# Kernel optimization log

Measured on AMD Instinct MI355X. Metric: run time of the kernel, lower is better.

The kernel has to match this reference:

```python
import jax, jax.numpy as jnp
import numpy as np

B, S, D, H, IT, V = 2, 1024, 1024, 8, 28, 50257
DH = D // H
EPS = jnp.float32(1.1920929e-07)  # torch RMSNorm default eps = finfo(float32).eps


def _rmsnorm(x, w):
    # torch nn.RMSNorm: x * rsqrt(mean(x^2) + eps) * weight
    ms = jnp.mean(jnp.square(x), axis=-1, keepdims=True)
    return x * jax.lax.rsqrt(ms + EPS) * w


def setup_inputs() -> dict:
    key = jax.random.key(0)
    ks = jax.random.split(key, 8)
    s = 0.02
    tokens = jax.random.randint(ks[0], (B, S), 0, V)
    embed = jax.random.normal(ks[1], (V, D), dtype=jnp.float32) * s
    Wk = jax.random.normal(ks[2], (D, D), dtype=jnp.float32) * s
    Wv = jax.random.normal(ks[3], (D, D), dtype=jnp.float32) * s
    Ws = jax.random.normal(ks[4], (D, D), dtype=jnp.float32) * s
    Wo = jax.random.normal(ks[5], (D, D), dtype=jnp.float32) * s  # original zero-inits; randomized for a non-trivial baseline
    step_size = jnp.linspace(0.5, 0.1, IT, dtype=jnp.float32)
    norm_w = jnp.ones((IT, D), jnp.float32)   # per-iteration RMSNorm weight
    gamma = jnp.ones((IT, D), jnp.float32)
    beta = jnp.zeros((IT, D), jnp.float32)
    out_norm_w = jnp.ones((D,), jnp.float32)
    lm_head_w = jax.random.normal(ks[6], (V, D), dtype=jnp.float32) * s
    return dict(tokens=tokens, embed=embed, Wk=Wk, Wv=Wv, Ws=Ws, Wo=Wo,
                step_size=step_size, norm_w=norm_w, gamma=gamma, beta=beta,
                out_norm_w=out_norm_w, lm_head_w=lm_head_w)


def _forward(tokens, embed, Wk, Wv, Ws, Wo, step_size, norm_w, gamma, beta, out_norm_w, lm_head_w):
    b, s = tokens.shape
    causal = jnp.tril(jnp.ones((s, s), dtype=bool))  # allow j <= i
    scale = 1.0 / np.sqrt(DH)

    def compute_force(h):
        k = (h @ Wk.T).reshape(b, s, H, DH)
        v = (h @ Wv.T).reshape(b, s, H, DH)
        energy = jnp.einsum('bihd,bjhd->bhij', k, k) * scale
        logits = jnp.where(causal, -energy, -jnp.inf)  # softmax(-energy) with causal masking
        w = jax.nn.softmax(logits, axis=-1)
        pairwise = jnp.einsum('bhij,bjhd->bihd', w, v).reshape(b, s, D)
        return (pairwise + h @ Ws.T) @ Wo.T

    def step(x, p):
        st, nw, g, bb = p
        h = _rmsnorm(x, nw) * g + bb
        return x + compute_force(h) * st, None

    x0 = embed[tokens].astype(jnp.float32)
    x, _ = jax.lax.scan(jax.checkpoint(step), x0, (step_size, norm_w, gamma, beta))
    x = _rmsnorm(x, out_norm_w)
    return x @ lm_head_w.T  # [B, S, V] logits


def reference(tokens, embed, Wk, Wv, Ws, Wo, step_size, norm_w, gamma, beta, out_norm_w, lm_head_w):
    return _forward(tokens, embed, Wk, Wv, Ws, Wo, step_size, norm_w, gamma, beta, out_norm_w, lm_head_w)
```

## Files before the change

kernel.cpp:

```cpp
#include <hip/hip_runtime.h>
#include <cstdint>
#include <cstddef>

#define S_   1024
#define D_   1024
#define H_   8
#define DH_  128
#define IT_  28
#define V_   50257
#define B_   2
#define ROWS 2048
#define EPS_ 1.1920929e-07f

typedef unsigned short u16;
typedef __attribute__((ext_vector_type(8))) short s8v;
typedef __attribute__((ext_vector_type(4))) float f4v;

static __device__ __forceinline__ void gload16(const void* g, void* l) {
  __builtin_amdgcn_global_load_lds((__attribute__((address_space(1))) void*)(g),
                                   (__attribute__((address_space(3))) void*)(l), 16, 0, 0);
}

static __device__ __forceinline__ u16 f2bf(float f) {
  union { float f; uint32_t u; } v; v.f = f;
  return (u16)((v.u + 0x7FFFu + ((v.u >> 16) & 1u)) >> 16);
}

static __device__ __forceinline__ float wave_sum(float v) {
#pragma unroll
  for (int o = 32; o > 0; o >>= 1) v += __shfl_xor(v, o, 64);
  return v;
}

__device__ __constant__ int IT_TAB[40] = {
  15,15,15,15, 14,14,14, 13,13,13, 12,12,12, 11,11,11,
  10,10, 9,9, 8,8, 7,7, 6, 5, 4, 3,
  14,10,6,2, 13,9,5,1, 12,8,4,0};
__device__ __constant__ int CH_TAB[40] = {
  0,1,2,3, 0,1,2, 0,1,2, 0,1,2, 0,1,2,
  0,1, 0,1, 0,1, 0,1, 0, 0, 0, 0,
  3,2,1,0, 3,2,1,0, 3,2,1,0};

__global__ __launch_bounds__(256) void k_embed(const int* __restrict__ tok,
                                               const float* __restrict__ emb,
                                               float* __restrict__ x) {
  const int row = blockIdx.x;
  const int t = tok[row];
  ((float4*)(x + (size_t)row * D_))[threadIdx.x] =
      ((const float4*)(emb + (size_t)t * D_))[threadIdx.x];
}

__global__ __launch_bounds__(256) void k_cvt(const float* __restrict__ w,
                                             u16* __restrict__ o, int n4) {
  const int idx = blockIdx.x * 256 + threadIdx.x;
  if (idx < n4) {
    const float4 f = ((const float4*)w)[idx];
    ushort4 u;
    u.x = f2bf(f.x); u.y = f2bf(f.y); u.z = f2bf(f.z); u.w = f2bf(f.w);
    ((ushort4*)o)[idx] = u;
  }
}

__global__ __launch_bounds__(256) void k_rmsnorm(const float* __restrict__ x,
                                                 const float* __restrict__ nw,
                                                 const float* __restrict__ g,
                                                 const float* __restrict__ bb,
                                                 u16* __restrict__ h) {
  const int row = blockIdx.x;
  const int tid = threadIdx.x;
  const float4 xv = ((const float4*)(x + (size_t)row * D_))[tid];
  float ss = xv.x*xv.x + xv.y*xv.y + xv.z*xv.z + xv.w*xv.w;
  ss = wave_sum(ss);
  __shared__ float red[4];
  const int lane = tid & 63, wid = tid >> 6;
  if (lane == 0) red[wid] = ss;
  __syncthreads();
  const float tot = red[0] + red[1] + red[2] + red[3];
  const float r = rsqrtf(tot * (1.0f / (float)D_) + EPS_);
  const float4 wv = ((const float4*)nw)[tid];
  float o[4];
  o[0] = xv.x * r * wv.x; o[1] = xv.y * r * wv.y;
  o[2] = xv.z * r * wv.z; o[3] = xv.w * r * wv.w;
  if (g) {
    const float4 gv = ((const float4*)g)[tid];
    const float4 bv = ((const float4*)bb)[tid];
    o[0] = o[0]*gv.x + bv.x; o[1] = o[1]*gv.y + bv.y;
    o[2] = o[2]*gv.z + bv.z; o[3] = o[3]*gv.w + bv.w;
  }
  ushort4 u;
  u.x = f2bf(o[0]); u.y = f2bf(o[1]); u.z = f2bf(o[2]); u.w = f2bf(o[3]);
  ((ushort4*)(h + (size_t)row * D_))[tid] = u;
}

template<int EPI, int SWAP>
__global__ __launch_bounds__(256) void k_gemm(const u16* __restrict__ A, int lda,
                                              const u16* __restrict__ Bm, int ldb,
                                              float* __restrict__ C, int ldc,
                                              int N, int K,
                                              const float* __restrict__ alphap, int aidx) {
  __shared__ u16 As[128 * 32];
  __shared__ u16 Bs[64 * 32];
  const int i0 = (SWAP ? blockIdx.x : blockIdx.y) * 128;
  const int j0 = (SWAP ? blockIdx.y : blockIdx.x) * 64;
  const int tid = threadIdx.x;
  const int lane = tid & 63, w = tid >> 6;
  const int wr = w >> 1, wc = w & 1;
  const int l15 = lane & 15, l4 = lane >> 4;
  const int ar = tid >> 2, ak = (tid & 3) << 3;
  int bj = j0 + ar; if (bj > N - 1) bj = N - 1;

  f4v acc[4][2];
#pragma unroll
  for (int m = 0; m < 4; ++m)
#pragma unroll
    for (int n = 0; n < 2; ++n) acc[m][n] = (f4v)0.0f;

  for (int k0 = 0; k0 < K; k0 += 32) {
    gload16(A + (size_t)(i0 + ar) * lda + k0 + ak, &As[(size_t)tid * 8]);
    gload16(A + (size_t)(i0 + ar + 64) * lda + k0 + ak, &As[((size_t)tid + 256) * 8]);
    gload16(Bm + (size_t)bj * ldb + k0 + ak, &Bs[(size_t)tid * 8]);
    __syncthreads();
    s8v a[4], b[2];
#pragma unroll
    for (int m = 0; m < 4; ++m)
      a[m] = *(const s8v*)&As[(wr * 64 + m * 16 + l15) * 32 + l4 * 8];
#pragma unroll
    for (int n = 0; n < 2; ++n)
      b[n] = *(const s8v*)&Bs[(wc * 32 + n * 16 + l15) * 32 + l4 * 8];
#pragma unroll
    for (int m = 0; m < 4; ++m)
#pragma unroll
      for (int n = 0; n < 2; ++n)
        acc[m][n] = __builtin_amdgcn_mfma_f32_16x16x32_bf16(a[m], b[n], acc[m][n], 0, 0, 0);
    __syncthreads();
  }

  const float alpha = alphap ? alphap[aidx] : 1.0f;
#pragma unroll
  for (int m = 0; m < 4; ++m) {
#pragma unroll
    for (int n = 0; n < 2; ++n) {
      const int i = i0 + wr * 64 + m * 16 + l4 * 4;
      const int j = j0 + wc * 32 + n * 16 + l15;
      const f4v v = acc[m][n];
      if (EPI == 0) {
        if (j < N) {
#pragma unroll
          for (int r = 0; r < 4; ++r) C[(size_t)(i + r) * ldc + j] = v[r];
        }
      } else {
#pragma unroll
        for (int r = 0; r < 4; ++r) C[(size_t)(i + r) * ldc + j] += alpha * v[r];
      }
    }
  }
}

__global__ __launch_bounds__(256) void k_gemm_qkv(const u16* __restrict__ A,
                                                  const u16* __restrict__ Wcat,
                                                  u16* __restrict__ kb,
                                                  u16* __restrict__ vt,
                                                  float* __restrict__ fb) {
  __shared__ u16 As[128 * 32];
  __shared__ u16 Bs[64 * 32];
  const int i0 = blockIdx.y * 128, j0 = blockIdx.x * 64;
  const int tid = threadIdx.x;
  const int lane = tid & 63, w = tid >> 6;
  const int wr = w >> 1, wc = w & 1;
  const int l15 = lane & 15, l4 = lane >> 4;
  const int ar = tid >> 2, ak = (tid & 3) << 3;

  f4v acc[4][2];
#pragma unroll
  for (int m = 0; m < 4; ++m)
#pragma unroll
    for (int n = 0; n < 2; ++n) acc[m][n] = (f4v)0.0f;

  for (int k0 = 0; k0 < D_; k0 += 32) {
    gload16(A + (size_t)(i0 + ar) * D_ + k0 + ak, &As[(size_t)tid * 8]);
    gload16(A + (size_t)(i0 + ar + 64) * D_ + k0 + ak, &As[((size_t)tid + 256) * 8]);
    gload16(Wcat + (size_t)(j0 + ar) * D_ + k0 + ak, &Bs[(size_t)tid * 8]);
    __syncthreads();
    s8v a[4], b[2];
#pragma unroll
    for (int m = 0; m < 4; ++m)
      a[m] = *(const s8v*)&As[(wr * 64 + m * 16 + l15) * 32 + l4 * 8];
#pragma unroll
    for (int n = 0; n < 2; ++n)
      b[n] = *(const s8v*)&Bs[(wc * 32 + n * 16 + l15) * 32 + l4 * 8];
#pragma unroll
    for (int m = 0; m < 4; ++m)
#pragma unroll
      for (int n = 0; n < 2; ++n)
        acc[m][n] = __builtin_amdgcn_mfma_f32_16x16x32_bf16(a[m], b[n], acc[m][n], 0, 0, 0);
    __syncthreads();
  }

#pragma unroll
  for (int m = 0; m < 4; ++m) {
#pragma unroll
    for (int n = 0; n < 2; ++n) {
      const int i = i0 + wr * 64 + m * 16 + l4 * 4;
      const int j = j0 + wc * 32 + n * 16 + l15;
      const int sel = j >> 10, jl = j & 1023;
      const f4v v = acc[m][n];
      if (sel == 0) {
#pragma unroll
        for (int r = 0; r < 4; ++r) kb[(size_t)(i + r) * D_ + jl] = f2bf(v[r]);
      } else if (sel == 1) {
        ushort4 p;
        p.x = f2bf(v[0]); p.y = f2bf(v[1]); p.z = f2bf(v[2]); p.w = f2bf(v[3]);
        *(ushort4*)&vt[((size_t)(i >> 10) * D_ + jl) * S_ + (i & 1023)] = p;
      } else {
#pragma unroll
        for (int r = 0; r < 4; ++r) fb[(size_t)(i + r) * D_ + jl] = v[r];
      }
    }
  }
}

__global__ __launch_bounds__(256) void k_attn_part(const u16* __restrict__ kb,
                                                   const u16* __restrict__ vt,
                                                   float* __restrict__ po,
                                                   float* __restrict__ pml,
                                                   float scale) {
  const int it = IT_TAB[blockIdx.x], ch = CH_TAB[blockIdx.x];
  const int z = blockIdx.y;
  const int b = z >> 3, h = z & 7;
  const u16* Kbh = kb + (size_t)b * S_ * D_ + h * DH_;
  const u16* Vth = vt + ((size_t)b * D_ + h * DH_) * S_;
  const int i0 = it * 64;
  const int jt0 = ch * 4;
  const int jtend = min(jt0 + 4, it + 1);
  __shared__ u16 Kj[64 * 128];
  __shared__ u16 Vj[128 * 64];
  __shared__ u16 Pl[4][16 * 64];
  const int tid = threadIdx.x;
  const int lane = tid & 63, w = tid >> 6;
  const int l15 = lane & 15, l4 = lane >> 4;

  s8v ka[4];
#pragma unroll
  for (int ks = 0; ks < 4; ++ks)
    ka[ks] = *(const s8v*)(Kbh + (size_t)(i0 + w * 16 + l15) * D_ + ks * 32 + l4 * 8);

  f4v acc_o[8];
#pragma unroll
  for (int n = 0; n < 8; ++n) acc_o[n] = (f4v)0.0f;
  float mrow[4], lrow[4];
#pragma unroll
  for (int r = 0; r < 4; ++r) { mrow[r] = -3.0e38f; lrow[r] = 0.f; }

  const int krow = tid >> 4, koff = (tid & 15) * 8;
  const int vrow = tid >> 3, voff = (tid & 7) * 8;

  for (int jt = jt0; jt < jtend; ++jt) {
    const int j0 = jt * 64;
#pragma unroll
    for (int p = 0; p < 4; ++p) {
      const int row = p * 16 + krow;
      gload16(Kbh + (size_t)(j0 + row) * D_ + (koff ^ ((row & 7) << 3)),
              &Kj[(size_t)(p * 256 + tid) * 8]);
    }
#pragma unroll
    for (int p = 0; p < 4; ++p) {
      const int row = p * 32 + vrow;
      gload16(Vth + (size_t)row * S_ + j0 + (voff ^ ((row & 7) << 3)),
              &Vj[(size_t)(p * 256 + tid) * 8]);
    }
    __syncthreads();

    f4v s[4];
#pragma unroll
    for (int n = 0; n < 4; ++n) s[n] = (f4v)0.0f;
#pragma unroll
    for (int ks = 0; ks < 4; ++ks) {
#pragma unroll
      for (int n = 0; n < 4; ++n) {
        const int row = n * 16 + l15;
        const s8v kf = *(const s8v*)&Kj[row * 128 + ((ks * 32 + l4 * 8) ^ ((row & 7) << 3))];
        s[n] = __builtin_amdgcn_mfma_f32_16x16x32_bf16(ka[ks], kf, s[n], 0, 0, 0);
      }
    }

    float pv[4][4], tmax[4];
#pragma unroll
    for (int r = 0; r < 4; ++r) tmax[r] = -3.0e38f;
#pragma unroll
    for (int n = 0; n < 4; ++n) {
      const int j = j0 + n * 16 + l15;
#pragma unroll
      for (int r = 0; r < 4; ++r) {
        const int i = i0 + w * 16 + l4 * 4 + r;
        const float lg = (j <= i) ? (-scale * s[n][r]) : -3.0e38f;
        pv[n][r] = lg;
        tmax[r] = fmaxf(tmax[r], lg);
      }
    }
#pragma unroll
    for (int r = 0; r < 4; ++r) {
#pragma unroll
      for (int o = 8; o > 0; o >>= 1) tmax[r] = fmaxf(tmax[r], __shfl_xor(tmax[r], o, 64));
    }
    float es[4];
#pragma unroll
    for (int r = 0; r < 4; ++r) {
      const float mn = fmaxf(mrow[r], tmax[r]);
      es[r] = __expf(mrow[r] - mn);
      mrow[r] = mn;
    }
    float psum[4] = {0.f, 0.f, 0.f, 0.f};
#pragma unroll
    for (int n = 0; n < 4; ++n) {
#pragma unroll
      for (int r = 0; r < 4; ++r) {
        const float p = __expf(pv[n][r] - mrow[r]);
        pv[n][r] = p;
        psum[r] += p;
      }
    }
#pragma unroll
    for (int r = 0; r < 4; ++r) {
#pragma unroll
      for (int o = 8; o > 0; o >>= 1) psum[r] += __shfl_xor(psum[r], o, 64);
      lrow[r] = lrow[r] * es[r] + psum[r];
    }
#pragma unroll
    for (int n = 0; n < 8; ++n) {
      f4v t = acc_o[n];
      t[0] *= es[0]; t[1] *= es[1]; t[2] *= es[2]; t[3] *= es[3];
      acc_o[n] = t;
    }

    u16* P = Pl[w];
#pragma unroll
    for (int n = 0; n < 4; ++n) {
#pragma unroll
      for (int r = 0; r < 4; ++r) {
        const int row = l4 * 4 + r;
        P[row * 64 + ((n * 16 + l15) ^ ((row & 7) << 3))] = f2bf(pv[n][r]);
      }
    }
    __syncthreads();
    s8v pa[2];
#pragma unroll
    for (int kp = 0; kp < 2; ++kp)
      pa[kp] = *(const s8v*)&P[l15 * 64 + ((kp * 32 + l4 * 8) ^ ((l15 & 7) << 3))];

#pragma unroll
    for (int kp = 0; kp < 2; ++kp) {
#pragma unroll
      for (int n = 0; n < 8; ++n) {
        const int d = n * 16 + l15;
        const s8v vf = *(const s8v*)&Vj[d * 64 + ((kp * 32 + l4 * 8) ^ ((d & 7) << 3))];
        acc_o[n] = __builtin_amdgcn_mfma_f32_16x16x32_bf16(pa[kp], vf, acc_o[n], 0, 0, 0);
      }
    }
    __syncthreads();
  }

  const int slot = (z * 16 + it) * 4 + ch;
  float* O = po + (size_t)slot * (64 * 128);
#pragma unroll
  for (int n = 0; n < 8; ++n) {
#pragma unroll
    for (int r = 0; r < 4; ++r)
      O[(w * 16 + l4 * 4 + r) * 128 + n * 16 + l15] = acc_o[n][r];
  }
  if (l15 == 0) {
#pragma unroll
    for (int r = 0; r < 4; ++r) {
      const int row = w * 16 + l4 * 4 + r;
      pml[(size_t)slot * 128 + row] = mrow[r];
      pml[(size_t)slot * 128 + 64 + row] = lrow[r];
    }
  }
}

__global__ __launch_bounds__(256) void k_attn_merge(const float* __restrict__ po,
                                                    const float* __restrict__ pml,
                                                    const float* __restrict__ fb,
                                                    u16* __restrict__ fbh) {
  const int it = blockIdx.x, z = blockIdx.y;
  const int b = z >> 3, h = z & 7;
  const int nch = (it >> 2) + 1;
  const int row = threadIdx.x >> 2;
  const int cseg = (threadIdx.x & 3) * 32;
  const int base = (z * 16 + it) * 4;

  float ms = -3.0e38f, mv[4], lv[4];
#pragma unroll
  for (int c = 0; c < 4; ++c)
    if (c < nch) {
      mv[c] = pml[(size_t)(base + c) * 128 + row];
      lv[c] = pml[(size_t)(base + c) * 128 + 64 + row];
      ms = fmaxf(ms, mv[c]);
    }
  float ls = 0.f, fac[4];
#pragma unroll
  for (int c = 0; c < 4; ++c)
    if (c < nch) { fac[c] = __expf(mv[c] - ms); ls += lv[c] * fac[c]; }
  const float inv = 1.0f / ls;

  float4 o[8];
#pragma unroll
  for (int q = 0; q < 8; ++q) o[q] = make_float4(0.f, 0.f, 0.f, 0.f);
#pragma unroll
  for (int c = 0; c < 4; ++c)
    if (c < nch) {
      const float4* Oc = (const float4*)(po + (size_t)(base + c) * (64 * 128) + row * 128 + cseg);
      const float f = fac[c];
#pragma unroll
      for (int q = 0; q < 8; ++q) {
        const float4 t = Oc[q];
        o[q].x += t.x * f; o[q].y += t.y * f; o[q].z += t.z * f; o[q].w += t.w * f;
      }
    }

  const size_t gidx = ((size_t)(b * S_ + it * 64 + row)) * D_ + h * DH_ + cseg;
  const float4* F = (const float4*)(fb + gidx);
  u16* out = fbh + gidx;
#pragma unroll
  for (int q = 0; q < 8; ++q) {
    const float4 fv = F[q];
    ushort4 u;
    u.x = f2bf(fv.x + o[q].x * inv);
    u.y = f2bf(fv.y + o[q].y * inv);
    u.z = f2bf(fv.z + o[q].z * inv);
    u.w = f2bf(fv.w + o[q].w * inv);
    *(ushort4*)(out + q * 4) = u;
  }
}

extern "C" void kernel_launch(void* const* d_in, const int* in_sizes, int n_in,
                              void* d_out, int out_size, void* d_ws, size_t ws_size,
                              hipStream_t stream) {
  const int*   tok = (const int*)  d_in[0];
  const float* emb = (const float*)d_in[1];
  const float* Wk  = (const float*)d_in[2];
  const float* Wv  = (const float*)d_in[3];
  const float* Ws  = (const float*)d_in[4];
  const float* Wo  = (const float*)d_in[5];
  const float* stp = (const float*)d_in[6];
  const float* nw  = (const float*)d_in[7];
  const float* gam = (const float*)d_in[8];
  const float* bet = (const float*)d_in[9];
  const float* onw = (const float*)d_in[10];
  const float* lmw = (const float*)d_in[11];
  float* out = (float*)d_out;

  uint8_t* wsb = (uint8_t*)d_ws;
  float* x   = (float*)wsb;  wsb += (size_t)ROWS * D_ * 4;
  u16* hb    = (u16*)wsb;    wsb += (size_t)ROWS * D_ * 2;
  u16* kb    = (u16*)wsb;    wsb += (size_t)ROWS * D_ * 2;
  u16* vt    = (u16*)wsb;    wsb += (size_t)ROWS * D_ * 2;
  float* fb  = (float*)wsb;  wsb += (size_t)ROWS * D_ * 4;
  u16* fbh   = (u16*)wsb;    wsb += (size_t)ROWS * D_ * 2;
  u16* Wcat  = (u16*)wsb;    wsb += (size_t)3 * D_ * D_ * 2;
  u16* Wob   = (u16*)wsb;    wsb += (size_t)D_ * D_ * 2;
  float* po  = (float*)wsb;  wsb += (size_t)1024 * 64 * 128 * 4;
  float* pml = (float*)wsb;  wsb += (size_t)1024 * 128 * 4;
  u16* Wlm   = (u16*)wsb;    wsb += (size_t)V_ * D_ * 2;

  const float scale = 0.08838834764831845f;
  const int n4 = D_ * D_ / 4;

  k_cvt<<<1024, 256, 0, stream>>>(Wk, Wcat, n4);
  k_cvt<<<1024, 256, 0, stream>>>(Wv, Wcat + (size_t)D_ * D_, n4);
  k_cvt<<<1024, 256, 0, stream>>>(Ws, Wcat + (size_t)2 * D_ * D_, n4);
  k_cvt<<<1024, 256, 0, stream>>>(Wo, Wob, n4);
  k_embed<<<ROWS, 256, 0, stream>>>(tok, emb, x);

  for (int it = 0; it < IT_; ++it) {
    k_rmsnorm<<<ROWS, 256, 0, stream>>>(x, nw + (size_t)it * D_,
                                        gam + (size_t)it * D_, bet + (size_t)it * D_, hb);
    k_gemm_qkv<<<dim3(48, 16), 256, 0, stream>>>(hb, Wcat, kb, vt, fb);
    k_attn_part<<<dim3(40, 16), 256, 0, stream>>>(kb, vt, po, pml, scale);
    k_attn_merge<<<dim3(16, 16), 256, 0, stream>>>(po, pml, fb, fbh);
    k_gemm<1, 0><<<dim3(16, 16), 256, 0, stream>>>(fbh, D_, Wob, D_, x, D_, D_, D_, stp, it);
  }

  k_rmsnorm<<<ROWS, 256, 0, stream>>>(x, onw, nullptr, nullptr, hb);

  k_cvt<<<(V_ * 256 + 255) / 256, 256, 0, stream>>>(lmw, Wlm, V_ * D_ / 4);
  k_gemm<0, 1><<<dim3(16, (V_ + 63) / 64), 256, 0, stream>>>(hb, D_, Wlm, D_, out, V_, V_, D_,
                                                             nullptr, 0);
}
```

Before: 2.927 ms.

## Widen LM-head GEMM tile to 128 columns and remap blocks per XCD

Adds a template parameter so the LM-head GEMM computes 128x128 tiles instead of 128x64. This halves how often the A operand is reloaded and doubles the MFMA work per LDS sync. For the swapped LM-head launch, it also remaps block IDs so consecutive tiles, which share the same B rows, land on the same XCD for better L2 reuse. The cost is more accumulator registers per thread and fewer blocks in the grid.

```diff
diff --git a/kernel.cpp b/kernel.cpp
--- a/kernel.cpp
+++ b/kernel.cpp
@@ -92,45 +92,57 @@
   ((ushort4*)(h + (size_t)row * D_))[tid] = u;
 }
 
-template<int EPI, int SWAP>
+template<int EPI, int SWAP, int NB>
 __global__ __launch_bounds__(256) void k_gemm(const u16* __restrict__ A, int lda,
                                               const u16* __restrict__ Bm, int ldb,
                                               float* __restrict__ C, int ldc,
                                               int N, int K,
                                               const float* __restrict__ alphap, int aidx) {
   __shared__ u16 As[128 * 32];
-  __shared__ u16 Bs[64 * 32];
-  const int i0 = (SWAP ? blockIdx.x : blockIdx.y) * 128;
-  const int j0 = (SWAP ? blockIdx.y : blockIdx.x) * 64;
+  __shared__ u16 Bs[64 * NB * 32];
+  int bid = blockIdx.x + gridDim.x * blockIdx.y;
+  if (SWAP) {
+    const int nwg = gridDim.x * gridDim.y;
+    const int q = nwg >> 3, r = nwg & 7;
+    const int xcd = bid & 7, lo = bid >> 3;
+    bid = (xcd < r ? xcd * (q + 1) : r * (q + 1) + (xcd - r) * q) + lo;
+  }
+  const int bx = bid % gridDim.x;
+  const int by = bid / gridDim.x;
+  const int i0 = (SWAP ? bx : by) * 128;
+  const int j0 = (SWAP ? by : bx) * (64 * NB);
   const int tid = threadIdx.x;
   const int lane = tid & 63, w = tid >> 6;
   const int wr = w >> 1, wc = w & 1;
   const int l15 = lane & 15, l4 = lane >> 4;
   const int ar = tid >> 2, ak = (tid & 3) << 3;
-  int bj = j0 + ar; if (bj > N - 1) bj = N - 1;
-
-  f4v acc[4][2];
+  int bj0 = j0 + ar;      if (bj0 > N - 1) bj0 = N - 1;
+  int bj1 = j0 + ar + 64; if (bj1 > N - 1) bj1 = N - 1;
+
+  f4v acc[4][2 * NB];
 #pragma unroll
   for (int m = 0; m < 4; ++m)
 #pragma unroll
-    for (int n = 0; n < 2; ++n) acc[m][n] = (f4v)0.0f;
+    for (int n = 0; n < 2 * NB; ++n) acc[m][n] = (f4v)0.0f;
 
   for (int k0 = 0; k0 < K; k0 += 32) {
     gload16(A + (size_t)(i0 + ar) * lda + k0 + ak, &As[(size_t)tid * 8]);
     gload16(A + (size_t)(i0 + ar + 64) * lda + k0 + ak, &As[((size_t)tid + 256) * 8]);
-    gload16(Bm + (size_t)bj * ldb + k0 + ak, &Bs[(size_t)tid * 8]);
-    __syncthreads();
-    s8v a[4], b[2];
+    gload16(Bm + (size_t)bj0 * ldb + k0 + ak, &Bs[(size_t)tid * 8]);
+    if (NB == 2)
+      gload16(Bm + (size_t)bj1 * ldb + k0 + ak, &Bs[((size_t)tid + 256) * 8]);
+    __syncthreads();
+    s8v a[4], b[2 * NB];
 #pragma unroll
     for (int m = 0; m < 4; ++m)
       a[m] = *(const s8v*)&As[(wr * 64 + m * 16 + l15) * 32 + l4 * 8];
 #pragma unroll
-    for (int n = 0; n < 2; ++n)
-      b[n] = *(const s8v*)&Bs[(wc * 32 + n * 16 + l15) * 32 + l4 * 8];
+    for (int n = 0; n < 2 * NB; ++n)
+      b[n] = *(const s8v*)&Bs[(wc * 32 * NB + n * 16 + l15) * 32 + l4 * 8];
 #pragma unroll
     for (int m = 0; m < 4; ++m)
 #pragma unroll
-      for (int n = 0; n < 2; ++n)
+      for (int n = 0; n < 2 * NB; ++n)
         acc[m][n] = __builtin_amdgcn_mfma_f32_16x16x32_bf16(a[m], b[n], acc[m][n], 0, 0, 0);
     __syncthreads();
   }
@@ -139,9 +151,9 @@
 #pragma unroll
   for (int m = 0; m < 4; ++m) {
 #pragma unroll
-    for (int n = 0; n < 2; ++n) {
+    for (int n = 0; n < 2 * NB; ++n) {
       const int i = i0 + wr * 64 + m * 16 + l4 * 4;
-      const int j = j0 + wc * 32 + n * 16 + l15;
+      const int j = j0 + wc * 32 * NB + n * 16 + l15;
       const f4v v = acc[m][n];
       if (EPI == 0) {
         if (j < N) {
@@ -477,12 +489,12 @@
     k_gemm_qkv<<<dim3(48, 16), 256, 0, stream>>>(hb, Wcat, kb, vt, fb);
     k_attn_part<<<dim3(40, 16), 256, 0, stream>>>(kb, vt, po, pml, scale);
     k_attn_merge<<<dim3(16, 16), 256, 0, stream>>>(po, pml, fb, fbh);
-    k_gemm<1, 0><<<dim3(16, 16), 256, 0, stream>>>(fbh, D_, Wob, D_, x, D_, D_, D_, stp, it);
+    k_gemm<1, 0, 1><<<dim3(16, 16), 256, 0, stream>>>(fbh, D_, Wob, D_, x, D_, D_, D_, stp, it);
   }
 
   k_rmsnorm<<<ROWS, 256, 0, stream>>>(x, onw, nullptr, nullptr, hb);
 
   k_cvt<<<(V_ * 256 + 255) / 256, 256, 0, stream>>>(lmw, Wlm, V_ * D_ / 4);
-  k_gemm<0, 1><<<dim3(16, (V_ + 63) / 64), 256, 0, stream>>>(hb, D_, Wlm, D_, out, V_, V_, D_,
-                                                             nullptr, 0);
-}
+  k_gemm<0, 1, 2><<<dim3(16, (V_ + 127) / 128), 256, 0, stream>>>(hb, D_, Wlm, D_, out, V_, V_, D_,
+                                                                  nullptr, 0);
+}
```

Result: no change. 2.914 ms (-0.5%).
